# Optimization experiments

Hardware: AMD Instinct MI355X
Metric: run time of the kernel (lower is better)

Reference implementation:

```python
import jax, jax.numpy as jnp
import numpy as np

N_HEAD = 16
NEG_INF = jnp.float32(-1e30)


def setup_inputs() -> dict:
    key = jax.random.key(0)
    k1, k2, k3 = jax.random.split(key, 3)
    B, T, C = 2, 2048, 1024
    x = jax.random.normal(k1, (B, T, C), dtype=jnp.float32)
    attn_mask = jnp.ones((B, T), dtype=jnp.int32)
    W_qkv = jax.random.normal(k2, (C, 3 * C), dtype=jnp.float32) * (1.0 / np.sqrt(C))
    b_qkv = jnp.zeros((3 * C,), dtype=jnp.float32)
    W_proj = jax.random.normal(k3, (C, C), dtype=jnp.float32) * (1.0 / np.sqrt(C))
    b_proj = jnp.zeros((C,), dtype=jnp.float32)
    return {"x": x, "attn_mask": attn_mask, "W_qkv": W_qkv, "b_qkv": b_qkv,
            "W_proj": W_proj, "b_proj": b_proj}


def reference(x, attn_mask, W_qkv, b_qkv, W_proj, b_proj):
    B, T, C = x.shape
    H = N_HEAD
    hd = C // H
    qkv = x @ W_qkv + b_qkv                       # [B,T,3C]
    q, k, v = jnp.split(qkv, 3, axis=-1)
    q = q.reshape(B, T, H, hd).transpose(0, 2, 1, 3)  # [B,H,T,hd]
    k = k.reshape(B, T, H, hd).transpose(0, 2, 1, 3)
    v = v.reshape(B, T, H, hd).transpose(0, 2, 1, 3)
    att = jnp.einsum('bhqd,bhkd->bhqk', q, k) / jnp.float32(np.sqrt(hd))  # [B,H,T,T]
    causal = jnp.tril(jnp.ones((T, T), dtype=bool))[None, None]           # [1,1,T,T]
    pad = (attn_mask != 0)[:, None, None, :]                              # [B,1,1,T]
    att = jnp.where(causal & pad, att, NEG_INF)
    att = jax.nn.softmax(att, axis=-1)
    y = jnp.einsum('bhqk,bhkd->bhqd', att, v)     # [B,H,T,hd]
    y = y.transpose(0, 2, 1, 3).reshape(B, T, C)
    return y @ W_proj + b_proj
```

## Files before the change

### kernel.cpp

```cpp
#include <hip/hip_runtime.h>

#define T_SEQ 2048
#define NHEAD 16
#define HD 64
#define CDIM 1024

typedef __bf16 bf16x8 __attribute__((ext_vector_type(8)));
typedef float f32x4 __attribute__((ext_vector_type(4)));
typedef float f32x16 __attribute__((ext_vector_type(16)));

union U16x8 { uint4 u4; unsigned short s[8]; bf16x8 b; };

__device__ __forceinline__ float bf2f(unsigned short u) {
    return __uint_as_float(((unsigned int)u) << 16);
}
__device__ __forceinline__ unsigned short f2bf(float f) {
    unsigned int u = __float_as_uint(f);
    u += 0x7fffu + ((u >> 16) & 1u);
    return (unsigned short)(u >> 16);
}
__device__ __forceinline__ U16x8 load8f(const float* __restrict__ p) {
    U16x8 r;
    float4 f0 = *(const float4*)p;
    float4 f1 = *(const float4*)(p + 4);
    r.s[0] = f2bf(f0.x); r.s[1] = f2bf(f0.y); r.s[2] = f2bf(f0.z); r.s[3] = f2bf(f0.w);
    r.s[4] = f2bf(f1.x); r.s[5] = f2bf(f1.y); r.s[6] = f2bf(f1.z); r.s[7] = f2bf(f1.w);
    return r;
}

__device__ __forceinline__ void async_copy16(const unsigned short* g, unsigned short* l) {
    __builtin_amdgcn_global_load_lds(
        (const __attribute__((address_space(1))) unsigned int*)g,
        (__attribute__((address_space(3))) unsigned int*)l, 16, 0, 0);
}

#define LOG2E 1.442695040f

#define BAR()    asm volatile("s_barrier" ::: "memory")
#define LGKM0()  asm volatile("s_waitcnt lgkmcnt(0)" ::: "memory")
#define VMC6()   asm volatile("s_waitcnt vmcnt(6)" ::: "memory")
#define VMC0()   asm volatile("s_waitcnt vmcnt(0)" ::: "memory")

__device__ __forceinline__ unsigned int cvtpk_bf16(float lo, float hi) {
    unsigned int r;
    asm("v_cvt_pk_bf16_f32 %0, %1, %2" : "=v"(r) : "v"(lo), "v"(hi));
    return r;
}
__device__ __forceinline__ void plane32swap(unsigned int &x, unsigned int &y) {
    asm("v_permlane32_swap_b32 %0, %1" : "+v"(x), "+v"(y));
}

__device__ __forceinline__ void transpose_tile(
    const float* __restrict__ in, unsigned short* __restrict__ out,
    int R, int C, int r0, int c0, float tile[64][65])
{
    const int tid = threadIdx.x;
    const int rr = tid >> 4;
    const int cc = (tid & 15) * 4;
#pragma unroll
    for (int p = 0; p < 4; ++p) {
        float4 v = *(const float4*)&in[(size_t)(r0 + p * 16 + rr) * C + c0 + cc];
        tile[p * 16 + rr][cc] = v.x;
        tile[p * 16 + rr][cc + 1] = v.y;
        tile[p * 16 + rr][cc + 2] = v.z;
        tile[p * 16 + rr][cc + 3] = v.w;
    }
    __syncthreads();
    const int n = tid >> 2;
    const int s = (tid & 3) * 8;
#pragma unroll
    for (int p = 0; p < 2; ++p) {
        const int k = s + p * 32;
        U16x8 o;
#pragma unroll
        for (int j = 0; j < 8; ++j) o.s[j] = f2bf(tile[k + j][n]);
        *(uint4*)&out[(size_t)(c0 + n) * R + r0 + k] = o.u4;
    }
}

__global__ __launch_bounds__(256) void prep(
    const float* __restrict__ X,     unsigned short* __restrict__ Xb,
    const float* __restrict__ Wqkv,  unsigned short* __restrict__ Wqkvt,
    const float* __restrict__ Wproj, unsigned short* __restrict__ Wprojt)
{
    __shared__ float tile[64][65];
    const int bid = blockIdx.x;
    if (bid < 2048) {
        const int i = (bid * 256 + threadIdx.x) * 8;
        U16x8 o = load8f(&X[i]);
        *(uint4*)&Xb[i] = o.u4;
    } else if (bid < 2816) {
        const int u = bid - 2048;
        transpose_tile(Wqkv, Wqkvt, CDIM, 3 * CDIM, (u & 15) * 64, (u >> 4) * 64, tile);
    } else {
        const int u = bid - 2816;
        transpose_tile(Wproj, Wprojt, CDIM, CDIM, (u & 15) * 64, (u >> 4) * 64, tile);
    }
}

__device__ __forceinline__ void gemm128_core(
    const unsigned short* __restrict__ A,
    const unsigned short* __restrict__ Bt,
    int K, int m0, int n0,
    unsigned short* As, unsigned short* Bs, f32x4 acc[4][4])
{
    const int tid = threadIdx.x;
    const int w = tid >> 6, lane = tid & 63;
    const int ln = lane & 15, quad = lane >> 4;
    const int wm = w >> 1, wn = w & 1;
    const int lr = lane >> 3;
    const int lc = (lane & 7) * 8;

    for (int kb = 0; kb < K; kb += 64) {
        __syncthreads();
#pragma unroll
        for (int i = 0; i < 4; ++i) {
            async_copy16(&A[(size_t)(m0 + w * 32 + i * 8 + lr) * K + kb + lc],
                         &As[(w * 32 + i * 8) * 64]);
            async_copy16(&Bt[(size_t)(n0 + w * 32 + i * 8 + lr) * K + kb + lc],
                         &Bs[(w * 32 + i * 8) * 64]);
        }
        __syncthreads();
#pragma unroll
        for (int kk = 0; kk < 2; ++kk) {
            U16x8 af[4], bff[4];
#pragma unroll
            for (int i = 0; i < 4; ++i)
                af[i].u4 = *(const uint4*)&As[(wm * 64 + i * 16 + ln) * 64 + kk * 32 + quad * 8];
#pragma unroll
            for (int j = 0; j < 4; ++j)
                bff[j].u4 = *(const uint4*)&Bs[(wn * 64 + j * 16 + ln) * 64 + kk * 32 + quad * 8];
#pragma unroll
            for (int i = 0; i < 4; ++i)
#pragma unroll
                for (int j = 0; j < 4; ++j)
                    acc[i][j] = __builtin_amdgcn_mfma_f32_16x16x32_bf16(af[i].b, bff[j].b, acc[i][j], 0, 0, 0);
        }
    }
}

__device__ __forceinline__ void stageA(const unsigned short* __restrict__ A,
                                       unsigned short* buf,
                                       int m0, int t, int unit, int w, int lane)
{
#pragma unroll
    for (int s = 0; s < 2; ++s) {
        const int r0 = s * 128 + unit * 64 + w * 8;
        const int row = r0 + (lane >> 3);
        const int col = (16 * (lane & 7)) ^ ((row & 4) ? 32 : 0);
        const unsigned short* src = A + (size_t)(m0 + row) * CDIM + t * 64 + (col >> 1);
        async_copy16(src, buf + r0 * 64);
    }
}

__device__ __forceinline__ void stageB(const unsigned short* __restrict__ B,
                                       unsigned short* buf,
                                       int n0, int t, int unit, int w, int lane)
{
#pragma unroll
    for (int s = 0; s < 2; ++s) {
        const int slice = s * 8 + w;
        const int r0 = (slice >> 2) * 64 + unit * 32 + (slice & 3) * 8;
        const int row = r0 + (lane >> 3);
        const int col = (16 * (lane & 7)) ^ ((row & 4) ? 32 : 0);
        const unsigned short* src = B + (size_t)(n0 + row) * CDIM + t * 64 + (col >> 1);
        async_copy16(src, buf + r0 * 64);
    }
}

__device__ __forceinline__ void readA(U16x8 af[4][2], const unsigned short* buf,
                                      int wm, int qm, int ln, int quad)
{
#pragma unroll
    for (int i = 0; i < 4; ++i) {
        const int row = wm * 128 + qm * 64 + i * 16 + ln;
        const int sw = (row & 4) ? 32 : 0;
#pragma unroll
        for (int kk = 0; kk < 2; ++kk) {
            const int byt = row * 128 + ((kk * 64 + quad * 16) ^ sw);
            af[i][kk].u4 = *(const uint4*)((const char*)buf + byt);
        }
    }
}

__device__ __forceinline__ void readB(U16x8 bf[2][2], const unsigned short* buf,
                                      int wn, int qn, int ln, int quad)
{
#pragma unroll
    for (int jj = 0; jj < 2; ++jj) {
        const int row = wn * 64 + qn * 32 + jj * 16 + ln;
        const int sw = (row & 4) ? 32 : 0;
#pragma unroll
        for (int kk = 0; kk < 2; ++kk) {
            const int byt = row * 128 + ((kk * 64 + quad * 16) ^ sw);
            bf[jj][kk].u4 = *(const uint4*)((const char*)buf + byt);
        }
    }
}

template<int QM, int QN>
__device__ __forceinline__ void mfma16(f32x4 acc[8][4], const U16x8 af[4][2],
                                       const U16x8 bf[2][2])
{
    __builtin_amdgcn_s_setprio(1);
#pragma unroll
    for (int i = 0; i < 4; ++i)
#pragma unroll
        for (int jj = 0; jj < 2; ++jj)
#pragma unroll
            for (int kk = 0; kk < 2; ++kk)
                acc[QM * 4 + i][QN * 2 + jj] = __builtin_amdgcn_mfma_f32_16x16x32_bf16(
                    af[i][kk].b, bf[jj][kk].b, acc[QM * 4 + i][QN * 2 + jj], 0, 0, 0);
    __builtin_amdgcn_s_setprio(0);
}

__global__ __launch_bounds__(512) void qkv8(
    const unsigned short* __restrict__ Xb,
    const unsigned short* __restrict__ Wt,
    const float* __restrict__ bias,
    unsigned short* __restrict__ Qp,
    unsigned short* __restrict__ Kp,
    unsigned short* __restrict__ Vtp)
{
    __shared__ __align__(1024) unsigned short smem[4][16384];
    unsigned short* Ab0 = smem[0];
    unsigned short* Ab1 = smem[1];
    unsigned short* Bb0 = smem[2];
    unsigned short* Bb1 = smem[3];

    const int tid = threadIdx.x;
    const int w = tid >> 6, lane = tid & 63;
    const int ln = lane & 15, quad = lane >> 4;
    const int wm = w >> 2, wn = w & 3;

    const int bid = blockIdx.x;
    const int swz = (bid & 7) * 24 + (bid >> 3);
    const int nt = swz % 12, mt = swz / 12;
    const int m0 = mt * 256, n0 = nt * 256;

    f32x4 acc[8][4];
#pragma unroll
    for (int i = 0; i < 8; ++i)
#pragma unroll
        for (int j = 0; j < 4; ++j) acc[i][j] = (f32x4){0.f, 0.f, 0.f, 0.f};

    stageA(Xb, Ab0, m0, 0, 0, w, lane);
    stageB(Wt, Bb0, n0, 0, 0, w, lane);
    stageB(Wt, Bb0, n0, 0, 1, w, lane);
    stageA(Xb, Ab0, m0, 0, 1, w, lane);
    stageA(Xb, Ab1, m0, 1, 0, w, lane);
    stageB(Wt, Bb1, n0, 1, 0, w, lane);
    stageB(Wt, Bb1, n0, 1, 1, w, lane);
    VMC6();
    BAR();

    U16x8 af[4][2], bq0[2][2], bq1[2][2];

    for (int j = 0; j < 7; ++j) {
        const int e = 2 * j, o = 2 * j + 1;
        readA(af, Ab0, wm, 0, ln, quad);
        readB(bq0, Bb0, wn, 0, ln, quad);
        stageA(Xb, Ab1, m0, o, 1, w, lane);
        BAR(); LGKM0();
        mfma16<0, 0>(acc, af, bq0);
        LGKM0(); BAR();
        readB(bq1, Bb0, wn, 1, ln, quad);
        stageA(Xb, Ab0, m0, e + 2, 0, w, lane);
        BAR(); LGKM0();
        mfma16<0, 1>(acc, af, bq1);
        LGKM0(); BAR();
        readA(af, Ab0, wm, 1, ln, quad);
        stageB(Wt, Bb0, n0, e + 2, 0, w, lane);
        BAR(); LGKM0();
        mfma16<1, 0>(acc, af, bq0);
        LGKM0(); BAR();
        stageB(Wt, Bb0, n0, e + 2, 1, w, lane);
        BAR();
        mfma16<1, 1>(acc, af, bq1);
        VMC6(); BAR();
        readA(af, Ab1, wm, 0, ln, quad);
        readB(bq0, Bb1, wn, 0, ln, quad);
        stageA(Xb, Ab0, m0, e + 2, 1, w, lane);
        BAR(); LGKM0();
        mfma16<0, 0>(acc, af, bq0);
        LGKM0(); BAR();
        readB(bq1, Bb1, wn, 1, ln, quad);
        stageA(Xb, Ab1, m0, o + 2, 0, w, lane);
        BAR(); LGKM0();
        mfma16<0, 1>(acc, af, bq1);
        LGKM0(); BAR();
        readA(af, Ab1, wm, 1, ln, quad);
        stageB(Wt, Bb1, n0, o + 2, 0, w, lane);
        BAR(); LGKM0();
        mfma16<1, 0>(acc, af, bq0);
        LGKM0(); BAR();
        stageB(Wt, Bb1, n0, o + 2, 1, w, lane);
        BAR();
        mfma16<1, 1>(acc, af, bq1);
        VMC6(); BAR();
    }

    stageA(Xb, Ab1, m0, 15, 1, w, lane);
    VMC0(); BAR();

    readA(af, Ab0, wm, 0, ln, quad);
    readB(bq0, Bb0, wn, 0, ln, quad);
    readB(bq1, Bb0, wn, 1, ln, quad);
    mfma16<0, 0>(acc, af, bq0);
    mfma16<0, 1>(acc, af, bq1);
    readA(af, Ab0, wm, 1, ln, quad);
    mfma16<1, 0>(acc, af, bq0);
    mfma16<1, 1>(acc, af, bq1);

    readA(af, Ab1, wm, 0, ln, quad);
    readB(bq0, Bb1, wn, 0, ln, quad);
    readB(bq1, Bb1, wn, 1, ln, quad);
    mfma16<0, 0>(acc, af, bq0);
    mfma16<0, 1>(acc, af, bq1);
    readA(af, Ab1, wm, 1, ln, quad);
    mfma16<1, 0>(acc, af, bq0);
    mfma16<1, 1>(acc, af, bq1);

    const int which = n0 >> 10;
    float bv[4];
#pragma unroll
    for (int jj = 0; jj < 4; ++jj) bv[jj] = bias[n0 + wn * 64 + jj * 16 + ln];

    if (which < 2) {
        unsigned short* dst = (which == 0) ? Qp : Kp;
        const float qsc = (which == 0) ? 0.125f : 1.0f;
#pragma unroll
        for (int jj = 0; jj < 4; ++jj) {
            const int n = n0 + wn * 64 + jj * 16 + ln;
            const int h = (n >> 6) & 15, d = n & 63;
#pragma unroll
            for (int i = 0; i < 8; ++i)
#pragma unroll
                for (int r = 0; r < 4; ++r) {
                    const int m = m0 + wm * 128 + i * 16 + quad * 4 + r;
                    const int b = m >> 11, tt = m & 2047;
                    dst[(((size_t)(b * NHEAD + h) * T_SEQ) + tt) * HD + d] =
                        f2bf((acc[i][jj][r] + bv[jj]) * qsc);
                }
        }
    } else {
#pragma unroll
        for (int jj = 0; jj < 4; ++jj) {
            const int n = n0 + wn * 64 + jj * 16 + ln;
            const int c = n - 2048;
#pragma unroll
            for (int i = 0; i < 8; ++i) {
                const int m00 = m0 + wm * 128 + i * 16 + quad * 4;
                const int b = m00 >> 11, tt = m00 & 2047;
                ushort4 pk;
                pk.x = f2bf(acc[i][jj][0] + bv[jj]);
                pk.y = f2bf(acc[i][jj][1] + bv[jj]);
                pk.z = f2bf(acc[i][jj][2] + bv[jj]);
                pk.w = f2bf(acc[i][jj][3] + bv[jj]);
                *(ushort4*)&Vtp[(size_t)(b * 1024 + c) * T_SEQ + tt] = pk;
            }
        }
    }
}

__global__ __launch_bounds__(256) void proj_gemm(
    const unsigned short* __restrict__ Yin,
    const unsigned short* __restrict__ Wt,
    const float* __restrict__ bias,
    float* __restrict__ out)
{
    __shared__ unsigned short As[128 * 64];
    __shared__ unsigned short Bs[128 * 64];
    const int m0 = blockIdx.y * 128;
    const int n0 = blockIdx.x * 128;

    f32x4 acc[4][4];
#pragma unroll
    for (int i = 0; i < 4; ++i)
#pragma unroll
        for (int j = 0; j < 4; ++j) acc[i][j] = (f32x4){0.f, 0.f, 0.f, 0.f};

    gemm128_core(Yin, Wt, CDIM, m0, n0, As, Bs, acc);

    const int tid = threadIdx.x;
    const int w = tid >> 6, lane = tid & 63;
    const int ln = lane & 15, quad = lane >> 4;
    const int wm = w >> 1, wn = w & 1;

#pragma unroll
    for (int j = 0; j < 4; ++j) {
        const int n = n0 + wn * 64 + j * 16 + ln;
        const float bv = bias[n];
#pragma unroll
        for (int i = 0; i < 4; ++i)
#pragma unroll
            for (int r = 0; r < 4; ++r) {
                const int m = m0 + wm * 64 + i * 16 + quad * 4 + r;
                out[(size_t)m * CDIM + n] = acc[i][j][r] + bv;
            }
    }
}


__device__ __forceinline__ int swz(int row, int slot) {
    return row * 64 + ((slot ^ (row & 7)) << 3);
}

__global__ __launch_bounds__(256) void flash_attn32(
    const unsigned short* __restrict__ Qp,
    const unsigned short* __restrict__ Kp,
    const unsigned short* __restrict__ Vtp,
    const int* __restrict__ mask,
    unsigned short* __restrict__ Y,
    unsigned short* __restrict__ Po,
    float* __restrict__ Pm,
    float* __restrict__ Pl)
{
    __shared__ unsigned short Ks[64 * 64];
    __shared__ unsigned short Vs[64 * 64];
    __shared__ float mask_arr[64];
    __shared__ float als[4][32];
    __shared__ int flagu;

    const int bh = blockIdx.x;
    const int y = blockIdx.y;
    int qb, j0, jstep;
    bool split;
    if (y < 16) { qb = 15 - (y >> 1); j0 = y & 1; jstep = 2; split = true; }
    else        { qb = 23 - y;        j0 = 0;     jstep = 1; split = false; }
    const int sgk = y & 1;

    const int b = bh >> 4, h = bh & 15;
    const int tid = threadIdx.x;
    const int w = tid >> 6, lane = tid & 63;
    const int l31 = lane & 31, hi = lane >> 5;
    const int row8 = tid >> 3, seg = tid & 7;
    const size_t base = (size_t)bh * T_SEQ * HD;
    const int qB = qb * 128;
    const int qw0 = qB + w * 32;
    const int qv = qw0 + l31;
    const int jlast = 2 * qb + 1;

    U16x8 qf[4];
    {
        const unsigned short* qrow = &Qp[base + (size_t)qv * HD];
#pragma unroll
        for (int c = 0; c < 4; ++c)
            qf[c].u4 = *(const uint4*)&qrow[c * 16 + hi * 8];
    }

    f32x16 oA0, oA1;
#pragma unroll
    for (int r = 0; r < 16; ++r) { oA0[r] = 0.f; oA1[r] = 0.f; }
    float m_r = -3.0e38f, mL = 0.f, l_r = 0.f;

    uint4 kr0, kr1, vr0, vr1;
    float mf = 0.f;
    {
        const unsigned short* kp0 = &Kp[base + (size_t)(j0 * 64 + row8) * HD + seg * 8];
        kr0 = *(const uint4*)kp0;
        kr1 = *(const uint4*)(kp0 + 32 * HD);
        const unsigned short* vp0 = &Vtp[base + (size_t)row8 * T_SEQ + j0 * 64 + seg * 8];
        vr0 = *(const uint4*)vp0;
        vr1 = *(const uint4*)(vp0 + 32 * T_SEQ);
        if (tid < 64) mf = mask[b * T_SEQ + j0 * 64 + tid] ? 0.f : -1.0e30f;
    }

    for (int j = j0; j <= jlast; j += jstep) {
        __syncthreads();
        *(uint4*)&Ks[swz(row8, seg)]      = kr0;
        *(uint4*)&Ks[swz(row8 + 32, seg)] = kr1;
        *(uint4*)&Vs[swz(row8, seg)]      = vr0;
        *(uint4*)&Vs[swz(row8 + 32, seg)] = vr1;
        if (w == 0) {
            const int k = lane;
            const int idx = ((k >> 2) & 1) * 32 + (k >> 5) * 16 + ((k & 31) >> 3) * 4 + (k & 3);
            mask_arr[idx] = mf;
            const unsigned long long bb = __ballot(mf == 0.f);
            if (lane == 0) flagu = (bb == 0xFFFFFFFFFFFFFFFFull) ? 0 : 1;
        }
        __syncthreads();

        const int jn = j + jstep;
        if (jn <= jlast) {
            const unsigned short* kp0 = &Kp[base + (size_t)(jn * 64 + row8) * HD + seg * 8];
            kr0 = *(const uint4*)kp0;
            kr1 = *(const uint4*)(kp0 + 32 * HD);
            const unsigned short* vp0 = &Vtp[base + (size_t)row8 * T_SEQ + jn * 64 + seg * 8];
            vr0 = *(const uint4*)vp0;
            vr1 = *(const uint4*)(vp0 + 32 * T_SEQ);
            if (tid < 64) mf = mask[b * T_SEQ + jn * 64 + tid] ? 0.f : -1.0e30f;
        }

        const bool skipw = (j * 64 > qw0 + 31);
        if (!skipw) {
            const bool edge = (j * 64 + 63 > qw0);
            const int anymask = flagu;

            f32x16 sc0, sc1;
#pragma unroll
            for (int r = 0; r < 16; ++r) { sc0[r] = 0.f; sc1[r] = 0.f; }
#pragma unroll
            for (int c = 0; c < 4; ++c) {
                U16x8 ka0, ka1;
                const int r0 = l31, r1 = 32 + l31;
                ka0.u4 = *(const uint4*)&Ks[r0 * 64 + (((2 * c + hi) ^ (r0 & 7)) << 3)];
                ka1.u4 = *(const uint4*)&Ks[r1 * 64 + (((2 * c + hi) ^ (r1 & 7)) << 3)];
                sc0 = __builtin_amdgcn_mfma_f32_32x32x16_bf16(ka0.b, qf[c].b, sc0, 0, 0, 0);
                sc1 = __builtin_amdgcn_mfma_f32_32x32x16_bf16(ka1.b, qf[c].b, sc1, 0, 0, 0);
            }

            if (anymask) {
#pragma unroll
                for (int g = 0; g < 4; ++g) {
                    const f32x4 m0v = *(const f32x4*)&mask_arr[hi * 32 + g * 4];
                    const f32x4 m1v = *(const f32x4*)&mask_arr[hi * 32 + 16 + g * 4];
#pragma unroll
                    for (int t = 0; t < 4; ++t) {
                        sc0[g * 4 + t] += m0v[t];
                        sc1[g * 4 + t] += m1v[t];
                    }
                }
            }
            if (edge) {
#pragma unroll
                for (int r = 0; r < 16; ++r) {
                    const int krow = (r & 3) + 8 * (r >> 2) + 4 * hi;
                    if (j * 64 + krow > qv)      sc0[r] = -1.0e30f;
                    if (j * 64 + 32 + krow > qv) sc1[r] = -1.0e30f;
                }
            }

            float tm = -3.0e38f;
#pragma unroll
            for (int r = 0; r < 16; ++r)
                tm = fmaxf(tm, fmaxf(sc0[r], sc1[r]));
            tm = fmaxf(tm, __shfl_xor(tm, 32));

            if (__any(tm > m_r + 8.f)) {
                const float mn = fmaxf(m_r, tm);
                const float a = __builtin_amdgcn_exp2f((m_r - mn) * LOG2E);
                m_r = mn; mL = mn * LOG2E;
                l_r *= a;
                if (hi == 0) als[w][l31] = a;
                f32x4 av[4];
#pragma unroll
                for (int g = 0; g < 4; ++g)
                    av[g] = *(const f32x4*)&als[w][g * 8 + hi * 4];
#pragma unroll
                for (int r = 0; r < 16; ++r) {
                    const float aa = av[r >> 2][r & 3];
                    oA0[r] *= aa; oA1[r] *= aa;
                }
            }

            float ps = 0.f;
#pragma unroll
            for (int r = 0; r < 16; ++r) {
                const float p0 = __builtin_amdgcn_exp2f(fmaf(sc0[r], LOG2E, -mL));
                const float p1 = __builtin_amdgcn_exp2f(fmaf(sc1[r], LOG2E, -mL));
                sc0[r] = p0; sc1[r] = p1;
                ps += p0 + p1;
            }
            l_r += ps;

#pragma unroll
            for (int c = 0; c < 4; ++c) {
                const int rb = (c & 1) * 8;
                unsigned int x0, y0, x1, y1;
                if (c < 2) {
                    x0 = cvtpk_bf16(sc0[rb + 0], sc0[rb + 1]);
                    y0 = cvtpk_bf16(sc0[rb + 4], sc0[rb + 5]);
                    x1 = cvtpk_bf16(sc0[rb + 2], sc0[rb + 3]);
                    y1 = cvtpk_bf16(sc0[rb + 6], sc0[rb + 7]);
                } else {
                    x0 = cvtpk_bf16(sc1[rb + 0], sc1[rb + 1]);
                    y0 = cvtpk_bf16(sc1[rb + 4], sc1[rb + 5]);
                    x1 = cvtpk_bf16(sc1[rb + 2], sc1[rb + 3]);
                    y1 = cvtpk_bf16(sc1[rb + 6], sc1[rb + 7]);
                }
                plane32swap(x0, y0);
                plane32swap(x1, y1);
                U16x8 pa;
                pa.u4 = make_uint4(x0, x1, y0, y1);
                {
                    const int vr_0 = l31, vr_1 = 32 + l31;
                    U16x8 vb0, vb1;
                    vb0.u4 = *(const uint4*)&Vs[vr_0 * 64 + (((2 * c + hi) ^ (vr_0 & 7)) << 3)];
                    vb1.u4 = *(const uint4*)&Vs[vr_1 * 64 + (((2 * c + hi) ^ (vr_1 & 7)) << 3)];
                    oA0 = __builtin_amdgcn_mfma_f32_32x32x16_bf16(pa.b, vb0.b, oA0, 0, 0, 0);
                    oA1 = __builtin_amdgcn_mfma_f32_32x32x16_bf16(pa.b, vb1.b, oA1, 0, 0, 0);
                }
            }
        }
    }

    const float lt = l_r + __shfl_xor(l_r, 32);

    if (split) {
        const int pidx = (bh * 8 + (qb - 8)) * 2 + sgk;
        if (hi == 0) {
            Pm[pidx * 128 + w * 32 + l31] = m_r;
            Pl[pidx * 128 + w * 32 + l31] = lt;
        }
#pragma unroll
        for (int r = 0; r < 16; ++r) {
            const int qlc = w * 32 + (r & 3) + 8 * (r >> 2) + 4 * hi;
            Po[(size_t)pidx * 8192 + qlc * 64 + l31]      = f2bf(oA0[r]);
            Po[(size_t)pidx * 8192 + qlc * 64 + 32 + l31] = f2bf(oA1[r]);
        }
    } else {
        if (hi == 0) als[w][l31] = 1.0f / lt;
        f32x4 lv[4];
#pragma unroll
        for (int g = 0; g < 4; ++g)
            lv[g] = *(const f32x4*)&als[w][g * 8 + hi * 4];
#pragma unroll
        for (int r = 0; r < 16; ++r) {
            const int q = qw0 + (r & 3) + 8 * (r >> 2) + 4 * hi;
            const float sl = lv[r >> 2][r & 3];
            const size_t row = (size_t)(b * T_SEQ + q);
            Y[row * CDIM + h * HD + l31]      = f2bf(oA0[r] * sl);
            Y[row * CDIM + h * HD + 32 + l31] = f2bf(oA1[r] * sl);
        }
    }
}

__global__ __launch_bounds__(256) void merge_attn(
    const unsigned short* __restrict__ Po,
    const float* __restrict__ Pm, const float* __restrict__ Pl,
    unsigned short* __restrict__ Y)
{
    const int u = blockIdx.x;
    const int bh = u & 31;
    const int v = u >> 5;
    const int qc = v >> 2, part = v & 3;
    const int tid = threadIdx.x;
    const int ql = part * 32 + (tid >> 3);
    const int d0 = (tid & 7) * 8;
    const int b = bh >> 4, h = bh & 15;
    const int i0 = (bh * 8 + qc) * 2, i1 = i0 + 1;

    const float m0 = Pm[i0 * 128 + ql], m1 = Pm[i1 * 128 + ql];
    const float l0 = Pl[i0 * 128 + ql], l1 = Pl[i1 * 128 + ql];
    const float M = fmaxf(m0, m1);
    const float f0 = __builtin_amdgcn_exp2f((m0 - M) * LOG2E);
    const float f1 = __builtin_amdgcn_exp2f((m1 - M) * LOG2E);
    const float inv = 1.0f / (f0 * l0 + f1 * l1);

    U16x8 a, c, o;
    a.u4 = *(const uint4*)&Po[(size_t)i0 * 8192 + ql * 64 + d0];
    c.u4 = *(const uint4*)&Po[(size_t)i1 * 8192 + ql * 64 + d0];
#pragma unroll
    for (int j = 0; j < 8; ++j)
        o.s[j] = f2bf((f0 * bf2f(a.s[j]) + f1 * bf2f(c.s[j])) * inv);

    const int q = 1024 + qc * 128 + ql;
    *(uint4*)&Y[(size_t)(b * T_SEQ + q) * CDIM + h * HD + d0] = o.u4;
}

extern "C" void kernel_launch(void* const* d_in, const int* in_sizes, int n_in,
                              void* d_out, int out_size, void* d_ws, size_t ws_size,
                              hipStream_t stream)
{
    const float* X     = (const float*)d_in[0];
    const int*   mask  = (const int*)d_in[1];
    const float* Wqkv  = (const float*)d_in[2];
    const float* bqkv  = (const float*)d_in[3];
    const float* Wproj = (const float*)d_in[4];
    const float* bproj = (const float*)d_in[5];
    float* out = (float*)d_out;

    const size_t per = (size_t)2 * NHEAD * T_SEQ * HD;
    unsigned short* Qp     = (unsigned short*)d_ws;
    unsigned short* Kp     = Qp + per;
    unsigned short* Vtp    = Kp + per;
    unsigned short* Xb     = Vtp + per;
    unsigned short* Yp     = Xb;
    unsigned short* Wqkvt  = Xb + per;
    unsigned short* Wprojt = Wqkvt + (size_t)3 * CDIM * CDIM;
    unsigned short* Po     = Wprojt + (size_t)CDIM * CDIM;
    float*          Pm     = (float*)(Po + (size_t)512 * 8192);
    float*          Pl     = Pm + 512 * 128;

    prep<<<3072, 256, 0, stream>>>(X, Xb, Wqkv, Wqkvt, Wproj, Wprojt);
    qkv8<<<192, 512, 0, stream>>>(Xb, Wqkvt, bqkv, Qp, Kp, Vtp);
    flash_attn32<<<dim3(2 * NHEAD, 24), 256, 0, stream>>>(Qp, Kp, Vtp, mask, Yp, Po, Pm, Pl);
    merge_attn<<<1024, 256, 0, stream>>>(Po, Pm, Pl, Yp);
    proj_gemm<<<dim3(8, 32), 256, 0, stream>>>(Yp, Wprojt, bproj, out);
}
```

Measured before the change: 214.7 us.

## Deepen flash-attention KV split to 4-way for late query blocks, 2-way for middle

The flash attention grid grows from 24 to 44 blocks per head. Query blocks 8-15 now split their KV range four ways, blocks 4-7 split two ways, and only blocks 0-3 run unsplit, which evens out per-block work under causal masking. The merge kernel now combines a variable number of partials (2 or 4) per query block and covers blocks 4-15. The partial buffers are made larger and placed over the Wqkv transpose region, which is dead by the time attention runs, so the extra workspace costs nothing. In exchange there is more partial-output traffic and a bigger merge pass.

```diff
diff --git a/kernel.cpp b/kernel.cpp
--- a/kernel.cpp
+++ b/kernel.cpp
@@ -426,9 +426,13 @@
     const int y = blockIdx.y;
     int qb, j0, jstep;
     bool split;
-    if (y < 16) { qb = 15 - (y >> 1); j0 = y & 1; jstep = 2; split = true; }
-    else        { qb = 23 - y;        j0 = 0;     jstep = 1; split = false; }
-    const int sgk = y & 1;
+    if (y < 32)      { qb = 15 - (y >> 2);        j0 = y & 3;        jstep = 4; split = true; }
+    else if (y < 40) { qb = 7 - ((y - 32) >> 1);  j0 = (y - 32) & 1; jstep = 2; split = true; }
+    else             { qb = 43 - y;               j0 = 0;            jstep = 1; split = false; }
+    const int pidx = split
+        ? ((qb < 8) ? (bh * 40 + (qb - 4) * 2 + j0)
+                    : (bh * 40 + 8 + (qb - 8) * 4 + j0))
+        : 0;
 
     const int b = bh >> 4, h = bh & 15;
     const int tid = threadIdx.x;
@@ -598,7 +602,6 @@
     const float lt = l_r + __shfl_xor(l_r, 32);
 
     if (split) {
-        const int pidx = (bh * 8 + (qb - 8)) * 2 + sgk;
         if (hi == 0) {
             Pm[pidx * 128 + w * 32 + l31] = m_r;
             Pl[pidx * 128 + w * 32 + l31] = lt;
@@ -634,29 +637,53 @@
     const int u = blockIdx.x;
     const int bh = u & 31;
     const int v = u >> 5;
-    const int qc = v >> 2, part = v & 3;
+    const int qb = 4 + (v >> 2), part = v & 3;
     const int tid = threadIdx.x;
     const int ql = part * 32 + (tid >> 3);
     const int d0 = (tid & 7) * 8;
     const int b = bh >> 4, h = bh & 15;
-    const int i0 = (bh * 8 + qc) * 2, i1 = i0 + 1;
-
-    const float m0 = Pm[i0 * 128 + ql], m1 = Pm[i1 * 128 + ql];
-    const float l0 = Pl[i0 * 128 + ql], l1 = Pl[i1 * 128 + ql];
-    const float M = fmaxf(m0, m1);
-    const float f0 = __builtin_amdgcn_exp2f((m0 - M) * LOG2E);
-    const float f1 = __builtin_amdgcn_exp2f((m1 - M) * LOG2E);
-    const float inv = 1.0f / (f0 * l0 + f1 * l1);
-
-    U16x8 a, c, o;
-    a.u4 = *(const uint4*)&Po[(size_t)i0 * 8192 + ql * 64 + d0];
-    c.u4 = *(const uint4*)&Po[(size_t)i1 * 8192 + ql * 64 + d0];
-#pragma unroll
-    for (int j = 0; j < 8; ++j)
-        o.s[j] = f2bf((f0 * bf2f(a.s[j]) + f1 * bf2f(c.s[j])) * inv);
-
-    const int q = 1024 + qc * 128 + ql;
-    *(uint4*)&Y[(size_t)(b * T_SEQ + q) * CDIM + h * HD + d0] = o.u4;
+
+    int S, basei;
+    if (qb < 8) { S = 2; basei = bh * 40 + (qb - 4) * 2; }
+    else        { S = 4; basei = bh * 40 + 8 + (qb - 8) * 4; }
+
+    float mv[4], lv[4];
+    float M = -3.0e38f;
+#pragma unroll
+    for (int s = 0; s < 4; ++s) {
+        if (s < S) {
+            mv[s] = Pm[(basei + s) * 128 + ql];
+            lv[s] = Pl[(basei + s) * 128 + ql];
+            M = fmaxf(M, mv[s]);
+        }
+    }
+    float f[4], L = 0.f;
+#pragma unroll
+    for (int s = 0; s < 4; ++s) {
+        if (s < S) {
+            f[s] = __builtin_amdgcn_exp2f((mv[s] - M) * LOG2E);
+            L += f[s] * lv[s];
+        }
+    }
+    const float inv = 1.0f / L;
+
+    float o[8] = {0.f, 0.f, 0.f, 0.f, 0.f, 0.f, 0.f, 0.f};
+#pragma unroll
+    for (int s = 0; s < 4; ++s) {
+        if (s < S) {
+            U16x8 a;
+            a.u4 = *(const uint4*)&Po[(size_t)(basei + s) * 8192 + ql * 64 + d0];
+#pragma unroll
+            for (int j = 0; j < 8; ++j) o[j] += f[s] * bf2f(a.s[j]);
+        }
+    }
+
+    U16x8 ot;
+#pragma unroll
+    for (int j = 0; j < 8; ++j) ot.s[j] = f2bf(o[j] * inv);
+
+    const int q = qb * 128 + ql;
+    *(uint4*)&Y[(size_t)(b * T_SEQ + q) * CDIM + h * HD + d0] = ot.u4;
 }
 
 extern "C" void kernel_launch(void* const* d_in, const int* in_sizes, int n_in,
@@ -677,15 +704,15 @@
     unsigned short* Vtp    = Kp + per;
     unsigned short* Xb     = Vtp + per;
     unsigned short* Yp     = Xb;
-    unsigned short* Wqkvt  = Xb + per;
-    unsigned short* Wprojt = Wqkvt + (size_t)3 * CDIM * CDIM;
-    unsigned short* Po     = Wprojt + (size_t)CDIM * CDIM;
-    float*          Pm     = (float*)(Po + (size_t)512 * 8192);
-    float*          Pl     = Pm + 512 * 128;
+    unsigned short* Wprojt = Xb + per;
+    unsigned short* Wqkvt  = Wprojt + (size_t)CDIM * CDIM;
+    unsigned short* Po     = Wqkvt;
+    float*          Pm     = (float*)(Po + (size_t)1280 * 8192);
+    float*          Pl     = Pm + 1280 * 128;
 
     prep<<<3072, 256, 0, stream>>>(X, Xb, Wqkv, Wqkvt, Wproj, Wprojt);
     qkv8<<<192, 512, 0, stream>>>(Xb, Wqkvt, bqkv, Qp, Kp, Vtp);
-    flash_attn32<<<dim3(2 * NHEAD, 24), 256, 0, stream>>>(Qp, Kp, Vtp, mask, Yp, Po, Pm, Pl);
-    merge_attn<<<1024, 256, 0, stream>>>(Po, Pm, Pl, Yp);
+    flash_attn32<<<dim3(2 * NHEAD, 44), 256, 0, stream>>>(Qp, Kp, Vtp, mask, Yp, Po, Pm, Pl);
+    merge_attn<<<1536, 256, 0, stream>>>(Po, Pm, Pl, Yp);
     proj_gemm<<<dim3(8, 32), 256, 0, stream>>>(Yp, Wprojt, bproj, out);
 }
```

After: 209.5 us. -2.4%, faster.
